# Performance work log

Measured on AMD Instinct MI355X. Metric: run time of the kernel, lower is better.

The kernel has to match this reference:

```python
import jax, jax.numpy as jnp
import numpy as np

B, T, D = 8, 2048, 1024
EPS = 1e-5

def _layernorm(x, g, b):
    mu = jnp.mean(x, axis=-1, keepdims=True)
    var = jnp.mean(jnp.square(x - mu), axis=-1, keepdims=True)
    return (x - mu) * jax.lax.rsqrt(var + EPS) * g + b

def setup_inputs() -> dict:
    key = jax.random.key(0)
    ks = jax.random.split(key, 8)
    scale = 1.0 / np.sqrt(D)
    text_inputs = jax.random.normal(ks[0], (B, T, D), dtype=jnp.float32)
    sit_mask = jax.random.randint(ks[1], (B, T), 0, 2).astype(jnp.float32)
    Wq = jax.random.normal(ks[2], (D, D), dtype=jnp.float32) * scale
    Wk = jax.random.normal(ks[3], (D, D), dtype=jnp.float32) * scale
    Wv = jax.random.normal(ks[4], (D, D), dtype=jnp.float32) * scale
    Wf1 = jax.random.normal(ks[5], (D, D), dtype=jnp.float32) * scale
    bf1 = jnp.zeros((D,), dtype=jnp.float32)
    Wf2 = jax.random.normal(ks[6], (D, D), dtype=jnp.float32) * scale
    bf2 = jnp.zeros((D,), dtype=jnp.float32)
    ln1_g = jnp.ones((D,), dtype=jnp.float32)
    ln1_b = jnp.zeros((D,), dtype=jnp.float32)
    ln2_g = jnp.ones((D,), dtype=jnp.float32)
    ln2_b = jnp.zeros((D,), dtype=jnp.float32)
    return dict(text_inputs=text_inputs, sit_mask=sit_mask, Wq=Wq, Wk=Wk, Wv=Wv,
                ln1_g=ln1_g, ln1_b=ln1_b, Wf1=Wf1, bf1=bf1, Wf2=Wf2, bf2=bf2,
                ln2_g=ln2_g, ln2_b=ln2_b)

def reference(text_inputs, sit_mask, Wq, Wk, Wv, ln1_g, ln1_b, Wf1, bf1, Wf2, bf2, ln2_g, ln2_b):
    x = text_inputs  # [B,T,D]
    d = x.shape[-1]
    # torch Linear: y = x @ W.T
    q = jnp.einsum('btd,ed->bte', x, Wq)
    k = jnp.einsum('btd,ed->bte', x, Wk)
    v = jnp.einsum('btd,ed->bte', x, Wv)
    # scaled scores with causal (strictly-upper = -inf) mask
    scores = jnp.einsum('btd,bsd->bts', q, k) / jnp.sqrt(jnp.asarray(d, x.dtype))
    causal = jnp.tril(jnp.ones((x.shape[1], x.shape[1]), dtype=bool))  # keep diag + past
    scores = jnp.where(causal[None], scores, -jnp.inf)
    attn = jax.nn.softmax(scores, axis=-1)
    # per-batch SIT padding mask applied AFTER softmax (rows may not sum to 1)
    pad_keep = (sit_mask[:, :, None] * sit_mask[:, None, :]) != 0  # [B,T,T]
    attn = jnp.where(pad_keep, attn, 0.0)
    att_out = jnp.einsum('bts,bsd->btd', attn, v)
    # residual + LN, FFN (Linear-ReLU-Linear), residual + LN
    h = _layernorm(att_out + x, ln1_g, ln1_b)
    ff = jnp.einsum('btd,ed->bte', jax.nn.relu(jnp.einsum('btd,ed->bte', h, Wf1) + bf1), Wf2) + bf2
    out = _layernorm(ff + h, ln2_g, ln2_b)
    return out
```

## Files before the change

kernel.cpp:

```cpp
#include <hip/hip_runtime.h>

typedef unsigned short ushort_t;
typedef __attribute__((ext_vector_type(8))) __bf16 bf16x8;
typedef __attribute__((ext_vector_type(4))) float f32x4;
typedef __attribute__((ext_vector_type(4))) int i32x4;
typedef __attribute__((ext_vector_type(4))) unsigned short u16x4;
typedef __attribute__((ext_vector_type(8))) unsigned short u16x8;

__device__ __forceinline__ float bf2f(ushort_t u) {
  union { unsigned u32; float f; } c; c.u32 = ((unsigned)u) << 16; return c.f;
}
__device__ __forceinline__ ushort_t f2bf(float f) {
  union { float f; unsigned u32; } c; c.f = f;
  unsigned u = c.u32;
  u += 0x7fffu + ((u >> 16) & 1u);
  return (ushort_t)(u >> 16);
}

__device__ __forceinline__ void gload_lds16(const void* g, void* l) {
  __builtin_amdgcn_global_load_lds(
      (const __attribute__((address_space(1))) void*)g,
      (__attribute__((address_space(3))) void*)l,
      16, 0, 0);
}

__device__ __forceinline__ void stage_half(const char* gbase, long row0, int ldbytes,
                                           int kbyte, char* lds_half, int tid)
{
  const int rl = tid >> 3;
  const int cs = ((tid & 7) ^ (rl & 7)) << 4;
  const char* g0 = gbase + (row0 + rl) * (long)ldbytes + kbyte + cs;
  char* l0 = lds_half + ((tid >> 6) << 10);
  gload_lds16(g0, l0);
  gload_lds16(g0 + (long)ldbytes * 64, l0 + 8192);
}

#define BAR() __builtin_amdgcn_s_barrier()
#define VMW6() asm volatile("s_waitcnt vmcnt(6)" ::: "memory")
#define VMW8() asm volatile("s_waitcnt vmcnt(8)" ::: "memory")
#define LGKM0() asm volatile("s_waitcnt lgkmcnt(0)" ::: "memory")
#define PR1() __builtin_amdgcn_s_setprio(1)
#define PR0() __builtin_amdgcn_s_setprio(0)

#define RD_A4(dst, base, rb) \
  _Pragma("unroll") for (int m_ = 0; m_ < 4; ++m_) { \
    const char* p_ = (base) + ((rb) + m_ * 16 + fr) * 128; \
    dst[m_][0] = *(const bf16x8*)(p_ + ch0); \
    dst[m_][1] = *(const bf16x8*)(p_ + ch1); }
#define RD_B2(dst, base, cb) \
  _Pragma("unroll") for (int n_ = 0; n_ < 2; ++n_) { \
    const char* p_ = (base) + ((cb) + n_ * 16 + fr) * 128; \
    dst[n_][0] = *(const bf16x8*)(p_ + ch0); \
    dst[n_][1] = *(const bf16x8*)(p_ + ch1); }

#define G_MM(ib, jb, Aa, Bb) \
  _Pragma("unroll") for (int m_ = 0; m_ < 4; ++m_) \
  _Pragma("unroll") for (int n_ = 0; n_ < 2; ++n_) \
  _Pragma("unroll") for (int s_ = 0; s_ < 2; ++s_) \
    acc[(ib) + m_][(jb) + n_] = __builtin_amdgcn_mfma_f32_16x16x32_bf16( \
        Aa[m_][s_], Bb[n_][s_], acc[(ib) + m_][(jb) + n_], 0, 0, 0);
#define SAE_(t, hh) stage_half(gA, m0 + (hh) * 128, ldab, (t) << 7, AE + (hh) * 16384, tid)
#define SAO_(t, hh) stage_half(gA, m0 + (hh) * 128, ldab, (t) << 7, AO + (hh) * 16384, tid)
#define SBE_(t, hh) stage_half(gB, n0 + (hh) * 128, ldbb, (t) << 7, BE + (hh) * 16384, tid)
#define SBO_(t, hh) stage_half(gB, n0 + (hh) * 128, ldbb, (t) << 7, BO + (hh) * 16384, tid)

template<int EPI, int MAPQ, bool ROUTE>
__global__ __launch_bounds__(512, 1) void gemm256(
    const ushort_t* __restrict__ A, int lda,
    const ushort_t* __restrict__ B, int ldb,
    ushort_t* __restrict__ C0, ushort_t* __restrict__ C1, ushort_t* __restrict__ C2,
    int ldc, const float* __restrict__ bias, float scale, int K)
{
  __shared__ __attribute__((aligned(16))) ushort_t lds[65536];

  int bx, by;
  if (MAPQ == 1) {
    const int flat = blockIdx.y * 4 + blockIdx.x;
    by = ((flat >> 5) << 3) | (flat & 7);
    bx = (flat >> 3) & 3;
  } else if (MAPQ == 2) {
    const int l = blockIdx.x;
    const int c = l & 7, u = l >> 3;
    const int q12 = u / 12;
    by = (q12 << 3) | c;
    bx = u - q12 * 12;
  } else { bx = blockIdx.x; by = blockIdx.y; }

  const int NT = K >> 6, NIT = NT >> 1, NTm1 = NT - 1;

  const int tid = threadIdx.x, lane = tid & 63;
  const int fr = lane & 15, g = lane >> 4, lm = lane & 7;
  const int wv = tid >> 6, wr = wv >> 2, wc = wv & 3;
  const int wrb = wr << 7, wcb = wc << 6;
  const long m0 = (long)by << 8, n0 = (long)bx << 8;

  const char* gA = (const char*)A;
  const char* gB = (const char*)B;
  const int ldab = lda << 1, ldbb = ldb << 1;

  const int ch0 = (g ^ lm) << 4;
  const int ch1 = ((4 | g) ^ lm) << 4;

  char* AE = (char*)lds;
  char* AO = AE + 32768;
  char* BE = AE + 65536;
  char* BO = AE + 98304;

  f32x4 acc[8][4] = {};
  bf16x8 aF[4][2], aG[4][2], bL[2][2], bL2[2][2], bH[2][2];

  SAE_(0, 0); SAE_(0, 1); SBE_(0, 0); SBE_(0, 1);
  SAO_(1, 0); SAO_(1, 1); SBO_(1, 0); SBO_(1, 1);
  VMW8(); BAR();
  RD_A4(aF, AE, wrb); RD_B2(bL, BE, wcb);

  for (int i = 0; i < NIT; ++i) {
    const int t2 = (2 * i + 2 < NTm1) ? 2 * i + 2 : NTm1;
    const int t3 = (2 * i + 3 < NTm1) ? 2 * i + 3 : NTm1;

    PR1(); G_MM(0, 0, aF, bL); PR0();
    RD_B2(bH, BE, wcb + 32);
    PR1(); G_MM(0, 2, aF, bH); PR0();
    RD_A4(aG, AE, wrb + 64);
    LGKM0(); BAR();
    PR1(); G_MM(4, 2, aG, bH); PR0();
    SAE_(t2, 0); SAE_(t2, 1); SBE_(t2, 0); SBE_(t2, 1);
    PR1(); G_MM(4, 0, aG, bL); PR0();
    VMW8(); BAR();
    RD_A4(aF, AO, wrb); RD_B2(bL2, BO, wcb);
    PR1(); G_MM(0, 0, aF, bL2); PR0();
    RD_B2(bH, BO, wcb + 32);
    PR1(); G_MM(0, 2, aF, bH); PR0();
    RD_A4(aG, AO, wrb + 64);
    LGKM0(); BAR();
    PR1(); G_MM(4, 2, aG, bH); PR0();
    SAO_(t3, 0); SAO_(t3, 1); SBO_(t3, 0); SBO_(t3, 1);
    PR1(); G_MM(4, 0, aG, bL2); PR0();
    VMW8(); BAR();
    RD_A4(aF, AE, wrb); RD_B2(bL, BE, wcb);
  }

  ushort_t* Cd = C0;
  long nc0 = (long)bx << 8;
  if constexpr (ROUTE) {
    const int which = bx >> 2;
    Cd = (which == 0) ? C0 : (which == 1) ? C1 : C2;
    nc0 = (long)(bx & 3) << 8;
  }

  const int cm = g << 2, cn = fr;
#pragma unroll
  for (int i2 = 0; i2 < 8; ++i2)
#pragma unroll
    for (int j2 = 0; j2 < 4; ++j2) {
      const long gm = m0 + wrb + i2 * 16 + cm;
      const long gn = nc0 + wcb + j2 * 16 + cn;
      float bv = 0.f;
      if constexpr (EPI >= 1) bv = bias[gn];
#pragma unroll
      for (int r = 0; r < 4; ++r) {
        float v = acc[i2][j2][r] * scale + bv;
        if constexpr (EPI == 2) v = fmaxf(v, 0.f);
        Cd[(gm + r) * ldc + gn] = f2bf(v);
      }
    }
}

#define A_MM(jb, Aa, Bb) \
  _Pragma("unroll") for (int m_ = 0; m_ < 4; ++m_) \
  _Pragma("unroll") for (int n_ = 0; n_ < 2; ++n_) \
  _Pragma("unroll") for (int s_ = 0; s_ < 2; ++s_) \
    acc[m_][(jb) + n_] = __builtin_amdgcn_mfma_f32_16x16x32_bf16( \
        Aa[m_][s_], Bb[n_][s_], acc[m_][(jb) + n_], 0, 0, 0);
#define SAA_(t, hh, dst) stage_half(gA, m0 + (hh) * 128, ldab, (t) << 7, (dst) + (hh) * 16384, tid)
#define SBA_(t, dst) stage_half(gB, n0, ldbb, (t) << 7, (dst), tid)

template<int EPI, int MAP, bool CKLIM>
__global__ __launch_bounds__(512, 1) void gemmA(
    const ushort_t* __restrict__ A, int lda, long bsA,
    const ushort_t* __restrict__ B, int ldb, long bsB,
    ushort_t* __restrict__ C, int ldc, long bsC,
    const float* __restrict__ bias, float scale, int K)
{
  __shared__ __attribute__((aligned(16))) ushort_t lds[73728];

  int bx, by, bz;
  if (MAP == 1) {
    const int bid = blockIdx.x;
    bz = bid & 7; const int r = bid >> 3;
    by = 0; while ((by + 1) * (by + 2) <= r) ++by;
    bx = r - by * (by + 1);
  } else if (MAP == 2) {
    const int bid = blockIdx.x;
    bz = bid & 7; const int u = bid >> 3;
    by = 7 - (u >> 3); bx = u & 7;
  } else { bx = blockIdx.x; by = blockIdx.y; bz = blockIdx.z; }

  const int NT = CKLIM ? ((by + 1) << 2) : (K >> 6);
  const int NIT = NT >> 1, NTm1 = NT - 1;

  const int tid = threadIdx.x, lane = tid & 63;
  const int fr = lane & 15, g = lane >> 4, lm = lane & 7;
  const int wv = tid >> 6, wr4 = wv >> 1, wc2 = wv & 1;
  const int wrb = wr4 << 6, wcb = wc2 << 6;
  const long m0 = (long)by << 8, n0 = (long)bx << 7;

  const char* gA = (const char*)(A + bz * bsA);
  const char* gB = (const char*)(B + bz * bsB);
  const int ldab = lda << 1, ldbb = ldb << 1;

  const int ch0 = (g ^ lm) << 4;
  const int ch1 = ((4 | g) ^ lm) << 4;

  char* pEA = (char*)lds;          char* pEB = pEA + 32768;
  char* pOA = (char*)lds + 49152;  char* pOB = pOA + 32768;
  char* pSA = (char*)lds + 98304;  char* pSB = pSA + 32768;

  f32x4 acc[4][4] = {};
  bf16x8 aE[4][2], aO[4][2], bLE[2][2], bLO[2][2], bH[2][2];

  SAA_(0, 0, pEA); SAA_(0, 1, pEA); SBA_(0, pEB);
  SAA_(1, 0, pOA); SAA_(1, 1, pOA); SBA_(1, pOB);
  VMW6(); BAR();
  RD_A4(aE, pEA, wrb); RD_B2(bLE, pEB, wcb);

  for (int i = 0; i < NIT; ++i) {
    const int t2 = (2 * i + 2 < NTm1) ? 2 * i + 2 : NTm1;
    const int t3 = (2 * i + 3 < NTm1) ? 2 * i + 3 : NTm1;

    PR1(); A_MM(0, aE, bLE); PR0();
    RD_B2(bH, pEB, wcb + 32);
    SAA_(t2, 0, pSA); SAA_(t2, 1, pSA); SBA_(t2, pSB);
    PR1(); A_MM(2, aE, bH); PR0();
    LGKM0(); VMW6(); BAR();
    RD_A4(aO, pOA, wrb); RD_B2(bLO, pOB, wcb);
    PR1(); A_MM(0, aO, bLO); PR0();
    RD_B2(bH, pOB, wcb + 32);
    SAA_(t3, 0, pEA); SAA_(t3, 1, pEA); SBA_(t3, pEB);
    PR1(); A_MM(2, aO, bH); PR0();
    LGKM0(); VMW6(); BAR();
    RD_A4(aE, pSA, wrb); RD_B2(bLE, pSB, wcb);
    char* tA = pEA; pEA = pSA; pSA = pOA; pOA = tA;
    char* tB = pEB; pEB = pSB; pSB = pOB; pOB = tB;
  }

  ushort_t* Cb = C + bz * bsC;
  const int cm = g << 2, cn = fr;
#pragma unroll
  for (int i2 = 0; i2 < 4; ++i2)
#pragma unroll
    for (int j2 = 0; j2 < 4; ++j2) {
      const long gm = m0 + wrb + i2 * 16 + cm;
      const long gn = n0 + wcb + j2 * 16 + cn;
      float bv = 0.f;
      if constexpr (EPI >= 1) bv = bias[gn];
#pragma unroll
      for (int r = 0; r < 4; ++r) {
        float v = acc[i2][j2][r] * scale + bv;
        if constexpr (EPI == 2) v = fmaxf(v, 0.f);
        Cb[(gm + r) * ldc + gn] = f2bf(v);
      }
    }
}

__global__ __launch_bounds__(256) void transpose_bf16(
    const ushort_t* __restrict__ V, int ldv, long bsV,
    ushort_t* __restrict__ Vt, int ldt, long bsT)
{
  __shared__ __attribute__((aligned(16))) ushort_t tile[64][72];
  const int bz = blockIdx.z;
  const ushort_t* Vb = V + bz * bsV;
  ushort_t* Tb = Vt + bz * bsT;
  const long s0 = (long)blockIdx.y << 6;
  const long d0 = (long)blockIdx.x << 6;
  const int tid = threadIdx.x;
  const int r = tid >> 3, c = tid & 7;
#pragma unroll
  for (int hh = 0; hh < 2; ++hh) {
    const int rr = r + hh * 32;
    i32x4 v = *(const i32x4*)(Vb + (s0 + rr) * ldv + d0 + c * 8);
    *(i32x4*)&tile[rr][c * 8] = v;
  }
  __syncthreads();
#pragma unroll
  for (int hh = 0; hh < 2; ++hh) {
    const int dr = r + hh * 32;
    union { ushort_t u[8]; i32x4 v; } t;
#pragma unroll
    for (int j = 0; j < 8; ++j) t.u[j] = tile[c * 8 + j][dr];
    *(i32x4*)(Tb + (d0 + dr) * ldt + s0 + c * 8) = t.v;
  }
}

__global__ __launch_bounds__(256) void softmax_sit2(ushort_t* __restrict__ S,
                                                    const float* __restrict__ sit)
{
  __shared__ float redA[4], redB[4];
  const int bid = blockIdx.x;
  const long rowA = bid, rowB = 16383 - bid;
  const int bA = (int)(rowA >> 11), tA = (int)(rowA & 2047);
  const int bB = (int)(rowB >> 11), tB = (int)(rowB & 2047);
  const int nA = tA + 1, nB = tB + 1;
  const int rupA = ((tA >> 8) + 1) << 8, rupB = ((tB >> 8) + 1) << 8;
  ushort_t* SrA = S + (rowA << 11);
  ushort_t* SrB = S + (rowB << 11);
  const int tid = threadIdx.x;
  const int i0 = tid << 3;
  const bool actA = i0 < rupA, actB = i0 < rupB;

  u16x8 rawA = {}, rawB = {};
  if (actA) rawA = *(const u16x8*)(SrA + i0);
  if (actB) rawB = *(const u16x8*)(SrB + i0);
  float vA[8], vB[8];
#pragma unroll
  for (int j = 0; j < 8; ++j) { vA[j] = bf2f(rawA[j]); vB[j] = bf2f(rawB[j]); }

  float mA = -3.0e38f, mB = -3.0e38f;
#pragma unroll
  for (int j = 0; j < 8; ++j) {
    if (i0 + j < nA) mA = fmaxf(mA, vA[j]);
    if (i0 + j < nB) mB = fmaxf(mB, vB[j]);
  }
#pragma unroll
  for (int o = 32; o > 0; o >>= 1) {
    mA = fmaxf(mA, __shfl_down(mA, o, 64));
    mB = fmaxf(mB, __shfl_down(mB, o, 64));
  }
  if ((tid & 63) == 0) { redA[tid >> 6] = mA; redB[tid >> 6] = mB; }
  __syncthreads();
  const float mxA = fmaxf(fmaxf(redA[0], redA[1]), fmaxf(redA[2], redA[3]));
  const float mxB = fmaxf(fmaxf(redB[0], redB[1]), fmaxf(redB[2], redB[3]));
  __syncthreads();

  float eA[8], eB[8];
  float sA = 0.f, sB = 0.f;
#pragma unroll
  for (int j = 0; j < 8; ++j) {
    eA[j] = (i0 + j < nA) ? __expf(vA[j] - mxA) : 0.f;
    eB[j] = (i0 + j < nB) ? __expf(vB[j] - mxB) : 0.f;
    sA += eA[j]; sB += eB[j];
  }
#pragma unroll
  for (int o = 32; o > 0; o >>= 1) {
    sA += __shfl_down(sA, o, 64);
    sB += __shfl_down(sB, o, 64);
  }
  if ((tid & 63) == 0) { redA[tid >> 6] = sA; redB[tid >> 6] = sB; }
  __syncthreads();
  const float lA = redA[0] + redA[1] + redA[2] + redA[3];
  const float lB = redB[0] + redB[1] + redB[2] + redB[3];

  float invA = 1.f / lA, invB = 1.f / lB;
  if (sit[rowA] == 0.f) invA = 0.f;
  if (sit[rowB] == 0.f) invB = 0.f;
  if (actA) {
    const float* sb = sit + ((long)bA << 11) + i0;
    u16x8 out;
#pragma unroll
    for (int j = 0; j < 8; ++j)
      out[j] = f2bf((i0 + j < nA && sb[j] != 0.f) ? eA[j] * invA : 0.f);
    *(u16x8*)(SrA + i0) = out;
  }
  if (actB) {
    const float* sb = sit + ((long)bB << 11) + i0;
    u16x8 out;
#pragma unroll
    for (int j = 0; j < 8; ++j)
      out[j] = f2bf((i0 + j < nB && sb[j] != 0.f) ? eB[j] * invB : 0.f);
    *(u16x8*)(SrB + i0) = out;
  }
}

template<bool RES_F32, bool OUT_F32>
__global__ __launch_bounds__(256) void resid_ln(
    const ushort_t* __restrict__ xin, const void* __restrict__ resv,
    const float* __restrict__ g, const float* __restrict__ be, void* __restrict__ outv)
{
  __shared__ float red[4];
  const long base = (long)blockIdx.x << 10;
  const int tid = threadIdx.x;
  const int i0 = tid << 2;

  const u16x4 xa = *(const u16x4*)(xin + base + i0);
  float v[4];
  if constexpr (RES_F32) {
    const float4 rv = *(const float4*)((const float*)resv + base + i0);
    v[0] = bf2f(xa.x) + rv.x; v[1] = bf2f(xa.y) + rv.y;
    v[2] = bf2f(xa.z) + rv.z; v[3] = bf2f(xa.w) + rv.w;
  } else {
    const u16x4 rb = *(const u16x4*)((const ushort_t*)resv + base + i0);
    v[0] = bf2f(xa.x) + bf2f(rb.x); v[1] = bf2f(xa.y) + bf2f(rb.y);
    v[2] = bf2f(xa.z) + bf2f(rb.z); v[3] = bf2f(xa.w) + bf2f(rb.w);
  }
  float s = v[0] + v[1] + v[2] + v[3];
#pragma unroll
  for (int o = 32; o > 0; o >>= 1) s += __shfl_down(s, o, 64);
  if ((tid & 63) == 0) red[tid >> 6] = s;
  __syncthreads();
  const float mu = (red[0] + red[1] + red[2] + red[3]) * (1.f / 1024.f);
  __syncthreads();
  float s2 = 0.f;
#pragma unroll
  for (int j = 0; j < 4; ++j) { const float d = v[j] - mu; s2 += d * d; }
#pragma unroll
  for (int o = 32; o > 0; o >>= 1) s2 += __shfl_down(s2, o, 64);
  if ((tid & 63) == 0) red[tid >> 6] = s2;
  __syncthreads();
  const float rstd = rsqrtf((red[0] + red[1] + red[2] + red[3]) * (1.f / 1024.f) + 1e-5f);

  const float4 gv = *(const float4*)(g + i0);
  const float4 bv = *(const float4*)(be + i0);
  const float o0 = (v[0] - mu) * rstd * gv.x + bv.x;
  const float o1 = (v[1] - mu) * rstd * gv.y + bv.y;
  const float o2 = (v[2] - mu) * rstd * gv.z + bv.z;
  const float o3 = (v[3] - mu) * rstd * gv.w + bv.w;
  if constexpr (OUT_F32) {
    float4 ov; ov.x = o0; ov.y = o1; ov.z = o2; ov.w = o3;
    *(float4*)((float*)outv + base + i0) = ov;
  } else {
    u16x4 ob = { f2bf(o0), f2bf(o1), f2bf(o2), f2bf(o3) };
    *(u16x4*)((ushort_t*)outv + base + i0) = ob;
  }
}

__global__ __launch_bounds__(256) void cast_f32_bf16(const float* __restrict__ src,
                                                     ushort_t* __restrict__ dst, int n4)
{
  const int i = blockIdx.x * 256 + threadIdx.x;
  if (i >= n4) return;
  const float4 v = *(const float4*)(src + ((long)i << 2));
  u16x4 o = { f2bf(v.x), f2bf(v.y), f2bf(v.z), f2bf(v.w) };
  *(u16x4*)(dst + ((long)i << 2)) = o;
}

__global__ __launch_bounds__(256) void cast_w5(
    const float* __restrict__ s0, const float* __restrict__ s1,
    const float* __restrict__ s2, const float* __restrict__ s3,
    const float* __restrict__ s4, ushort_t* __restrict__ dst)
{
  const int w = blockIdx.y;
  const float* src = (w == 0) ? s0 : (w == 1) ? s1 : (w == 2) ? s2 : (w == 3) ? s3 : s4;
  const long off = (long)w << 20;
  const int i = blockIdx.x * 256 + threadIdx.x;
  const float4 v = *(const float4*)(src + ((long)i << 2));
  u16x4 o = { f2bf(v.x), f2bf(v.y), f2bf(v.z), f2bf(v.w) };
  *(u16x4*)(dst + off + ((long)i << 2)) = o;
}

extern "C" void kernel_launch(void* const* d_in, const int* in_sizes, int n_in,
                              void* d_out, int out_size, void* d_ws, size_t ws_size,
                              hipStream_t stream) {
  const int T = 2048, D = 1024;
  const long TD = (long)T * D;
  const long ND = 8 * TD;
  const float* x    = (const float*)d_in[0];
  const float* sit  = (const float*)d_in[1];
  const float* Wq   = (const float*)d_in[2];
  const float* Wk   = (const float*)d_in[3];
  const float* Wv   = (const float*)d_in[4];
  const float* ln1g = (const float*)d_in[5];
  const float* ln1b = (const float*)d_in[6];
  const float* Wf1  = (const float*)d_in[7];
  const float* bf1  = (const float*)d_in[8];
  const float* Wf2  = (const float*)d_in[9];
  const float* bf2  = (const float*)d_in[10];
  const float* ln2g = (const float*)d_in[11];
  const float* ln2b = (const float*)d_in[12];

  ushort_t* W16 = (ushort_t*)d_ws;
  ushort_t* xb  = W16;
  ushort_t* vb  = W16 + ND;
  ushort_t* S   = W16;
  ushort_t* hb  = W16;
  ushort_t* ff1 = W16 + ND;
  ushort_t* vt  = W16 + 2 * ND;
  ushort_t* ff2 = vt;
  ushort_t* wq  = W16 + 3 * ND;
  ushort_t* wf1 = wq + 3L * D * D;
  ushort_t* wf2 = wf1 + (long)D * D;
  ushort_t* qb = (ushort_t*)d_out;
  ushort_t* kb = qb + ND;
  ushort_t* attb = (ushort_t*)d_out;

  cast_f32_bf16<<<16384, 256, 0, stream>>>(x, xb, (int)(ND / 4));
  cast_w5<<<dim3(1024, 5), 256, 0, stream>>>(Wq, Wk, Wv, Wf1, Wf2, wq);

  gemm256<0, 2, true><<<dim3(768), 512, 0, stream>>>(
      xb, 1024, wq, 1024, qb, kb, vb, 1024, nullptr, 1.f, 1024);

  transpose_bf16<<<dim3(16, 32, 8), 256, 0, stream>>>(vb, 1024, TD, vt, 2048, TD);

  gemmA<0, 1, false><<<dim3(576), 512, 0, stream>>>(
      qb, 1024, TD, kb, 1024, TD, S, 2048, (long)T * T, nullptr, 0.03125f, 1024);

  softmax_sit2<<<8192, 256, 0, stream>>>(S, sit);

  gemmA<0, 2, true><<<dim3(512), 512, 0, stream>>>(
      S, 2048, (long)T * T, vt, 2048, TD, attb, 1024, TD, nullptr, 1.f, 2048);

  resid_ln<true, false><<<16384, 256, 0, stream>>>(attb, x, ln1g, ln1b, hb);

  gemm256<2, 1, false><<<dim3(4, 64), 512, 0, stream>>>(
      hb, 1024, wf1, 1024, ff1, ff1, ff1, 1024, bf1, 1.f, 1024);
  gemm256<1, 1, false><<<dim3(4, 64), 512, 0, stream>>>(
      ff1, 1024, wf2, 1024, ff2, ff2, ff2, 1024, bf2, 1.f, 1024);

  resid_ln<false, true><<<16384, 256, 0, stream>>>(ff2, hb, ln2g, ln2b, (float*)d_out);
}
```

Baseline: 392.6 us.

## Restructure gemm256 to four waves with 128x128 per-wave tiles

The 256x256 GEMM block moves from 8 waves (each 128x64) to 4 waves (each 128x128, 64 accumulators). Staging now uses a 4-load-per-thread loader, and the interleaved prefetch/compute schedule becomes a simpler load-all-fragments-then-compute pattern, with global staging issued after each barrier. This raises per-wave reuse of A/B fragments and cuts LDS reads per MFMA. The cost is much higher register pressure and fewer waves to hide latency, and the staging of the next tile no longer overlaps the MFMA work.

```diff
diff --git a/kernel.cpp b/kernel.cpp
--- a/kernel.cpp
+++ b/kernel.cpp
@@ -35,9 +35,23 @@
   gload_lds16(g0 + (long)ldbytes * 64, l0 + 8192);
 }
 
+__device__ __forceinline__ void stage128(const char* gbase, long row0, int ldbytes,
+                                         int kbyte, char* lds_buf, int tid)
+{
+  const int rl = tid >> 3;
+  const int w = tid >> 6;
+#pragma unroll
+  for (int k = 0; k < 4; ++k) {
+    const int row = rl + k * 32;
+    const int cs = ((tid & 7) ^ (row & 7)) << 4;
+    const char* g0 = gbase + (row0 + row) * (long)ldbytes + kbyte + cs;
+    gload_lds16(g0, lds_buf + k * 4096 + w * 1024);
+  }
+}
+
 #define BAR() __builtin_amdgcn_s_barrier()
 #define VMW6() asm volatile("s_waitcnt vmcnt(6)" ::: "memory")
-#define VMW8() asm volatile("s_waitcnt vmcnt(8)" ::: "memory")
+#define VMW16() asm volatile("s_waitcnt vmcnt(16)" ::: "memory")
 #define LGKM0() asm volatile("s_waitcnt lgkmcnt(0)" ::: "memory")
 #define PR1() __builtin_amdgcn_s_setprio(1)
 #define PR0() __builtin_amdgcn_s_setprio(0)
@@ -53,19 +67,29 @@
     dst[n_][0] = *(const bf16x8*)(p_ + ch0); \
     dst[n_][1] = *(const bf16x8*)(p_ + ch1); }
 
-#define G_MM(ib, jb, Aa, Bb) \
-  _Pragma("unroll") for (int m_ = 0; m_ < 4; ++m_) \
-  _Pragma("unroll") for (int n_ = 0; n_ < 2; ++n_) \
+#define Q_RA(dst, base) \
+  _Pragma("unroll") for (int m_ = 0; m_ < 8; ++m_) { \
+    const char* p_ = (base) + (wrb + m_ * 16 + fr) * 128; \
+    dst[m_][0] = *(const bf16x8*)(p_ + ch0); \
+    dst[m_][1] = *(const bf16x8*)(p_ + ch1); }
+#define Q_RB(dst, base, cb) \
+  _Pragma("unroll") for (int n_ = 0; n_ < 4; ++n_) { \
+    const char* p_ = (base) + ((cb) + n_ * 16 + fr) * 128; \
+    dst[n_][0] = *(const bf16x8*)(p_ + ch0); \
+    dst[n_][1] = *(const bf16x8*)(p_ + ch1); }
+#define Q_MM(jb, Bb) \
+  _Pragma("unroll") for (int m_ = 0; m_ < 8; ++m_) \
+  _Pragma("unroll") for (int n_ = 0; n_ < 4; ++n_) \
   _Pragma("unroll") for (int s_ = 0; s_ < 2; ++s_) \
-    acc[(ib) + m_][(jb) + n_] = __builtin_amdgcn_mfma_f32_16x16x32_bf16( \
-        Aa[m_][s_], Bb[n_][s_], acc[(ib) + m_][(jb) + n_], 0, 0, 0);
-#define SAE_(t, hh) stage_half(gA, m0 + (hh) * 128, ldab, (t) << 7, AE + (hh) * 16384, tid)
-#define SAO_(t, hh) stage_half(gA, m0 + (hh) * 128, ldab, (t) << 7, AO + (hh) * 16384, tid)
-#define SBE_(t, hh) stage_half(gB, n0 + (hh) * 128, ldbb, (t) << 7, BE + (hh) * 16384, tid)
-#define SBO_(t, hh) stage_half(gB, n0 + (hh) * 128, ldbb, (t) << 7, BO + (hh) * 16384, tid)
+    acc[m_][(jb) + n_] = __builtin_amdgcn_mfma_f32_16x16x32_bf16( \
+        aF[m_][s_], Bb[n_][s_], acc[m_][(jb) + n_], 0, 0, 0);
+#define STGA(t, buf) do { stage128(gA, m0, ldab, (t) << 7, (buf), tid); \
+    stage128(gA, m0 + 128, ldab, (t) << 7, (buf) + 16384, tid); } while (0)
+#define STGB(t, buf) do { stage128(gB, n0, ldbb, (t) << 7, (buf), tid); \
+    stage128(gB, n0 + 128, ldbb, (t) << 7, (buf) + 16384, tid); } while (0)
 
 template<int EPI, int MAPQ, bool ROUTE>
-__global__ __launch_bounds__(512, 1) void gemm256(
+__global__ __launch_bounds__(256, 1) void gemm256(
     const ushort_t* __restrict__ A, int lda,
     const ushort_t* __restrict__ B, int ldb,
     ushort_t* __restrict__ C0, ushort_t* __restrict__ C1, ushort_t* __restrict__ C2,
@@ -90,8 +114,9 @@
 
   const int tid = threadIdx.x, lane = tid & 63;
   const int fr = lane & 15, g = lane >> 4, lm = lane & 7;
-  const int wv = tid >> 6, wr = wv >> 2, wc = wv & 3;
-  const int wrb = wr << 7, wcb = wc << 6;
+  const int wv = tid >> 6;
+  const int wr = wv >> 1, wc = wv & 1;
+  const int wrb = wr << 7, wcb = wc << 7;
   const long m0 = (long)by << 8, n0 = (long)bx << 8;
 
   const char* gA = (const char*)A;
@@ -106,38 +131,33 @@
   char* BE = AE + 65536;
   char* BO = AE + 98304;
 
-  f32x4 acc[8][4] = {};
-  bf16x8 aF[4][2], aG[4][2], bL[2][2], bL2[2][2], bH[2][2];
-
-  SAE_(0, 0); SAE_(0, 1); SBE_(0, 0); SBE_(0, 1);
-  SAO_(1, 0); SAO_(1, 1); SBO_(1, 0); SBO_(1, 1);
-  VMW8(); BAR();
-  RD_A4(aF, AE, wrb); RD_B2(bL, BE, wcb);
+  f32x4 acc[8][8] = {};
+  bf16x8 aF[8][2], bX[4][2], bY[4][2];
+
+  STGA(0, AE); STGB(0, BE);
+  STGA(1, AO); STGB(1, BO);
+  VMW16(); BAR();
 
   for (int i = 0; i < NIT; ++i) {
     const int t2 = (2 * i + 2 < NTm1) ? 2 * i + 2 : NTm1;
     const int t3 = (2 * i + 3 < NTm1) ? 2 * i + 3 : NTm1;
 
-    PR1(); G_MM(0, 0, aF, bL); PR0();
-    RD_B2(bH, BE, wcb + 32);
-    PR1(); G_MM(0, 2, aF, bH); PR0();
-    RD_A4(aG, AE, wrb + 64);
+    Q_RA(aF, AE);
+    Q_RB(bX, BE, wcb);
+    PR1(); Q_MM(0, bX); PR0();
+    Q_RB(bY, BE, wcb + 64);
+    PR1(); Q_MM(4, bY); PR0();
     LGKM0(); BAR();
-    PR1(); G_MM(4, 2, aG, bH); PR0();
-    SAE_(t2, 0); SAE_(t2, 1); SBE_(t2, 0); SBE_(t2, 1);
-    PR1(); G_MM(4, 0, aG, bL); PR0();
-    VMW8(); BAR();
-    RD_A4(aF, AO, wrb); RD_B2(bL2, BO, wcb);
-    PR1(); G_MM(0, 0, aF, bL2); PR0();
-    RD_B2(bH, BO, wcb + 32);
-    PR1(); G_MM(0, 2, aF, bH); PR0();
-    RD_A4(aG, AO, wrb + 64);
+    STGA(t2, AE); STGB(t2, BE);
+    VMW16(); BAR();
+    Q_RA(aF, AO);
+    Q_RB(bX, BO, wcb);
+    PR1(); Q_MM(0, bX); PR0();
+    Q_RB(bY, BO, wcb + 64);
+    PR1(); Q_MM(4, bY); PR0();
     LGKM0(); BAR();
-    PR1(); G_MM(4, 2, aG, bH); PR0();
-    SAO_(t3, 0); SAO_(t3, 1); SBO_(t3, 0); SBO_(t3, 1);
-    PR1(); G_MM(4, 0, aG, bL2); PR0();
-    VMW8(); BAR();
-    RD_A4(aF, AE, wrb); RD_B2(bL, BE, wcb);
+    STGA(t3, AO); STGB(t3, BO);
+    VMW16(); BAR();
   }
 
   ushort_t* Cd = C0;
@@ -152,7 +172,7 @@
 #pragma unroll
   for (int i2 = 0; i2 < 8; ++i2)
 #pragma unroll
-    for (int j2 = 0; j2 < 4; ++j2) {
+    for (int j2 = 0; j2 < 8; ++j2) {
       const long gm = m0 + wrb + i2 * 16 + cm;
       const long gn = nc0 + wcb + j2 * 16 + cn;
       float bv = 0.f;
@@ -485,7 +505,7 @@
   cast_f32_bf16<<<16384, 256, 0, stream>>>(x, xb, (int)(ND / 4));
   cast_w5<<<dim3(1024, 5), 256, 0, stream>>>(Wq, Wk, Wv, Wf1, Wf2, wq);
 
-  gemm256<0, 2, true><<<dim3(768), 512, 0, stream>>>(
+  gemm256<0, 2, true><<<dim3(768), 256, 0, stream>>>(
       xb, 1024, wq, 1024, qb, kb, vb, 1024, nullptr, 1.f, 1024);
 
   transpose_bf16<<<dim3(16, 32, 8), 256, 0, stream>>>(vb, 1024, TD, vt, 2048, TD);
@@ -500,9 +520,9 @@
 
   resid_ln<true, false><<<16384, 256, 0, stream>>>(attb, x, ln1g, ln1b, hb);
 
-  gemm256<2, 1, false><<<dim3(4, 64), 512, 0, stream>>>(
+  gemm256<2, 1, false><<<dim3(4, 64), 256, 0, stream>>>(
       hb, 1024, wf1, 1024, ff1, ff1, ff1, 1024, bf1, 1.f, 1024);
-  gemm256<1, 1, false><<<dim3(4, 64), 512, 0, stream>>>(
+  gemm256<1, 1, false><<<dim3(4, 64), 256, 0, stream>>>(
       ff1, 1024, wf2, 1024, ff2, ff2, ff2, 1024, bf2, 1.f, 1024);
 
   resid_ln<false, true><<<16384, 256, 0, stream>>>(ff2, hb, ln2g, ln2b, (float*)d_out);
```

After: 595.2 us. +51.6%, slower.
